# Kernel optimization log

Measured on AMD Instinct MI355X. Metric: run time of the kernel, lower is better.

## Reference

```python
import jax, jax.numpy as jnp
import numpy as np

HIDDEN = 4096
NUM_HEADS = 32
NUM_KV_HEADS = 8
HEAD_DIM = HIDDEN // NUM_HEADS  # 128
GROUPS = NUM_HEADS // NUM_KV_HEADS  # 4
ROPE_THETA = 10000.0


def setup_inputs() -> dict:
    key = jax.random.key(0)
    k0, k1, k2, k3, k4 = jax.random.split(key, 5)
    b, s = 2, 2048
    hidden_states = jax.random.normal(k0, (b, s, HIDDEN), dtype=jnp.float32)
    position_ids = jnp.broadcast_to(jnp.arange(s, dtype=jnp.int64), (b, s))
    sc = 1.0 / np.sqrt(HIDDEN)
    Wq = jax.random.normal(k1, (HIDDEN, NUM_HEADS * HEAD_DIM), dtype=jnp.float32) * sc
    Wk = jax.random.normal(k2, (HIDDEN, NUM_KV_HEADS * HEAD_DIM), dtype=jnp.float32) * sc
    Wv = jax.random.normal(k3, (HIDDEN, NUM_KV_HEADS * HEAD_DIM), dtype=jnp.float32) * sc
    Wo = jax.random.normal(k4, (NUM_HEADS * HEAD_DIM, HIDDEN), dtype=jnp.float32) * sc
    return {"hidden_states": hidden_states, "position_ids": position_ids,
            "Wq": Wq, "Wk": Wk, "Wv": Wv, "Wo": Wo}


def _rope(x, cos, sin):
    # x: [b, s, h, d]; cos/sin: [b, s, 1, d]
    d2 = x.shape[-1] // 2
    x1, x2 = x[..., :d2], x[..., d2:]
    rot = jnp.concatenate([-x2, x1], axis=-1)
    return x * cos + rot * sin


def reference(hidden_states, position_ids, Wq, Wk, Wv, Wo):
    b, s, _ = hidden_states.shape
    scale = 1.0 / np.sqrt(HEAD_DIM)
    # projections (Linear, no bias) kept in [b, s, h, d] layout
    q = (hidden_states @ Wq).reshape(b, s, NUM_HEADS, HEAD_DIM)
    k = (hidden_states @ Wk).reshape(b, s, NUM_KV_HEADS, HEAD_DIM)
    v = (hidden_states @ Wv).reshape(b, s, NUM_KV_HEADS, HEAD_DIM)
    # RoPE: emb = cat(freqs, freqs)
    inv_freq = 1.0 / (ROPE_THETA ** (jnp.arange(0, HEAD_DIM, 2, dtype=jnp.float32) / HEAD_DIM))
    freqs = position_ids.astype(jnp.float32)[..., None] * inv_freq  # [b, s, d/2]
    emb = jnp.concatenate([freqs, freqs], axis=-1)[:, :, None, :]   # [b, s, 1, d]
    cos, sin = jnp.cos(emb), jnp.sin(emb)
    q = _rope(q, cos, sin)
    k = _rope(k, cos, sin)
    # GQA: query head h maps to kv head h // GROUPS (repeat_kv is contiguous expand)
    qg = q.reshape(b, s, NUM_KV_HEADS, GROUPS, HEAD_DIM)
    scores = jnp.einsum('bqkgd,bskd->bkgqs', qg, k) * scale  # [b, kv, g, s_q, s_k]
    probs = jax.nn.softmax(scores, axis=-1)
    out = jnp.einsum('bkgqs,bskd->bqkgd', probs, v).reshape(b, s, HIDDEN)
    return out @ Wo
```

## Files before the change

### kernel.cpp

```cpp
#include <hip/hip_runtime.h>

typedef unsigned short u16;
typedef unsigned int u32;
typedef __attribute__((ext_vector_type(8))) __bf16 bf16x8;
typedef __attribute__((ext_vector_type(4))) float f32x4;
typedef __attribute__((ext_vector_type(4))) u32 u32x4;

__device__ __forceinline__ u16 f2bf(float f) {
  union { float f; u32 u; } v; v.f = f;
  u32 r = v.u + 0x7fffu + ((v.u >> 16) & 1u);
  return (u16)(r >> 16);
}
__device__ __forceinline__ float bf2f(u16 h) {
  return __uint_as_float(((u32)h) << 16);
}
__device__ __forceinline__ u32 pk2(float a, float b) {
  return (u32)f2bf(a) | ((u32)f2bf(b) << 16);
}
__device__ __forceinline__ void gld16(void* lds, const void* g) {
  __builtin_amdgcn_global_load_lds(
      (__attribute__((address_space(1))) void*)g,
      (__attribute__((address_space(3))) void*)lds, 16, 0, 0);
}

__global__ void convert_x(const float* __restrict__ src, u16* __restrict__ dst) {
  const size_t c = (size_t)blockIdx.x * blockDim.x + threadIdx.x;
  const float* s = src + c * 8;
  u16 t[8];
#pragma unroll
  for (int i = 0; i < 8; ++i) t[i] = f2bf(s[i]);
  ((uint4*)dst)[c] = *(const uint4*)t;
}

__global__ void transpose_w(const float* __restrict__ srcf, u16* __restrict__ dst,
                            int K, int N) {
  __shared__ u16 tile[64][72];
  const int r0 = blockIdx.y * 64, c0 = blockIdx.x * 64;
  const int tr = threadIdx.x >> 2;
  const int tc = (threadIdx.x & 3) * 16;
  const float* src = srcf + (size_t)(r0 + tr) * N + c0 + tc;
  u16* t = &tile[tr][tc];
#pragma unroll
  for (int i = 0; i < 16; ++i) t[i] = f2bf(src[i]);
  __syncthreads();
  u16 tmp[16];
#pragma unroll
  for (int i = 0; i < 16; ++i) tmp[i] = tile[tc + i][tr];
  uint4* gd = (uint4*)(dst + (size_t)(c0 + tr) * K + r0 + tc);
  gd[0] = *(uint4*)&tmp[0];
  gd[1] = *(uint4*)&tmp[8];
}

__global__ void transpose_v(const u16* __restrict__ V, u16* __restrict__ Vt) {
  __shared__ u16 tile[64][72];
  const int z = blockIdx.z, b = z >> 3, h = z & 7;
  const int s0 = blockIdx.y * 64;
  const int d0 = blockIdx.x * 64;
  const u16* src = V + ((size_t)(b * 2048 + s0)) * 1024 + h * 128 + d0;
  u16* dst = Vt + ((size_t)((b * 8 + h) * 128 + d0)) * 2048 + s0;
  const int tr = threadIdx.x >> 2;
  const int tc = (threadIdx.x & 3) * 16;
  const uint4* gs = (const uint4*)(src + (size_t)tr * 1024 + tc);
  *(uint4*)&tile[tr][tc] = gs[0];
  *(uint4*)&tile[tr][tc + 8] = gs[1];
  __syncthreads();
  u16 tmp[16];
#pragma unroll
  for (int i = 0; i < 16; ++i) tmp[i] = tile[tc + i][tr];
  uint4* gd = (uint4*)(dst + (size_t)tr * 2048 + tc);
  gd[0] = *(uint4*)&tmp[0];
  gd[1] = *(uint4*)&tmp[8];
}

template <int OUT32>
__global__ __launch_bounds__(256, 2) void gemm_bt128(
    const u16* __restrict__ A, const u16* __restrict__ Bt,
    void* __restrict__ Cv, int K, int N) {
  __shared__ u16 As[128 * 64];
  __shared__ u16 Bs[128 * 64];
  const int tid = threadIdx.x;
  const int wave = tid >> 6, lane = tid & 63;
  const int m0 = blockIdx.y * 128, n0 = blockIdx.x * 128;
  const int wr = (wave >> 1) * 64, wc = (wave & 1) * 64;
  const int lrow = lane & 15, quad = lane >> 4;
  const int cbase = wave * 64 + lane;

  f32x4 acc[4][4];
#pragma unroll
  for (int i = 0; i < 4; ++i)
#pragma unroll
    for (int j = 0; j < 4; ++j) acc[i][j] = (f32x4){0.f, 0.f, 0.f, 0.f};

  for (int k0 = 0; k0 < K; k0 += 64) {
#pragma unroll
    for (int r = 0; r < 4; ++r) {
      const int c = r * 256 + cbase;
      const int row = c >> 3, col = (c & 7) * 8;
      gld16(&As[(size_t)(r * 4 + wave) * 512],
            A + (size_t)(m0 + row) * K + k0 + col);
      gld16(&Bs[(size_t)(r * 4 + wave) * 512],
            Bt + (size_t)(n0 + row) * K + k0 + col);
    }
    __syncthreads();
#pragma unroll
    for (int kk = 0; kk < 2; ++kk) {
      const int ko = kk * 32 + quad * 8;
      bf16x8 af[4], bfr[4];
#pragma unroll
      for (int i = 0; i < 4; ++i)
        af[i] = *(const bf16x8*)&As[(wr + i * 16 + lrow) * 64 + ko];
#pragma unroll
      for (int j = 0; j < 4; ++j)
        bfr[j] = *(const bf16x8*)&Bs[(wc + j * 16 + lrow) * 64 + ko];
#pragma unroll
      for (int i = 0; i < 4; ++i)
#pragma unroll
        for (int j = 0; j < 4; ++j)
          acc[i][j] = __builtin_amdgcn_mfma_f32_16x16x32_bf16(af[i], bfr[j], acc[i][j], 0, 0, 0);
    }
    __syncthreads();
  }
#pragma unroll
  for (int i = 0; i < 4; ++i)
#pragma unroll
    for (int j = 0; j < 4; ++j)
#pragma unroll
      for (int reg = 0; reg < 4; ++reg) {
        const int row = m0 + wr + i * 16 + quad * 4 + reg;
        const int col = n0 + wc + j * 16 + lrow;
        if (OUT32)
          ((float*)Cv)[(size_t)row * N + col] = acc[i][j][reg];
        else
          ((u16*)Cv)[(size_t)row * N + col] = f2bf(acc[i][j][reg]);
      }
}

__global__ void rope_kernel(u16* __restrict__ Q, u16* __restrict__ Kc) {
  const int row = blockIdx.x;
  const float p = (float)(row & 2047);
  const float csc = 0.088388347762774597f * 1.4426950408889634f;
  for (int t = threadIdx.x; t < 2560; t += 256) {
    u16* base;
    int d;
    float sc;
    if (t < 2048) { const int h = t >> 6; d = t & 63; base = Q + (size_t)row * 4096 + h * 128; sc = csc; }
    else { const int tt = t - 2048; const int h = tt >> 6; d = tt & 63; base = Kc + (size_t)row * 1024 + h * 128; sc = 1.f; }
    const float inv = exp2f((float)d * -0.20762050593046807f);
    const float f = p * inv;
    float s, c;
    sincosf(f, &s, &c);
    const float x1 = bf2f(base[d]);
    const float x2 = bf2f(base[d + 64]);
    base[d] = f2bf((x1 * c - x2 * s) * sc);
    base[d + 64] = f2bf((x2 * c + x1 * s) * sc);
  }
}

__global__ __launch_bounds__(256, 3) void attn(
    const u16* __restrict__ Q, const u16* __restrict__ Kc,
    const u16* __restrict__ Vt, u16* __restrict__ O) {
  __shared__ u16 smem[16384];
  u16* Qs = smem;
  u16* Ks = smem;
  u16* Vs = smem + 8192;
  const int tid = threadIdx.x, wave = tid >> 6, lane = tid & 63;
  const int qt = blockIdx.x, qh = blockIdx.y, b = blockIdx.z;
  const int kvh = qh >> 2;
  const int lrow = lane & 15, quad = lane >> 4;
  const int swz = (lrow & 7) << 3;

  const u16* qb = Q + ((size_t)(b * 2048 + qt * 128)) * 4096 + qh * 128;
#pragma unroll
  for (int r = 0; r < 8; ++r) {
    const int c = (r * 4 + wave) * 64 + lane;
    const int row = c >> 4, scol = (c & 15) ^ (row & 7);
    gld16(&Qs[(size_t)(r * 4 + wave) * 512],
          qb + (size_t)row * 4096 + scol * 8);
  }
  __syncthreads();
  bf16x8 aq[2][4];
#pragma unroll
  for (int i = 0; i < 2; ++i)
#pragma unroll
    for (int kk = 0; kk < 4; ++kk)
      aq[i][kk] = *(const bf16x8*)
          &Qs[(wave * 32 + i * 16 + lrow) * 128 + ((kk * 32 + quad * 8) ^ swz)];
  __syncthreads();

  {
    const u16* kb = Kc + ((size_t)(b * 2048)) * 1024 + kvh * 128;
#pragma unroll
    for (int r = 0; r < 4; ++r) {
      const int c = (r * 4 + wave) * 64 + lane;
      const int m = c >> 4, scol = (c & 15) ^ (m & 7);
      const int srcrow = ((m >> 5) << 5) | (((m >> 2) & 3) << 3) |
                         (((m >> 4) & 1) << 2) | (m & 3);
      gld16(&Ks[(size_t)(r * 4 + wave) * 512],
            kb + (size_t)srcrow * 1024 + scol * 8);
    }
  }
  __syncthreads();

  f32x4 acco[2][8];
#pragma unroll
  for (int i = 0; i < 2; ++i)
#pragma unroll
    for (int j = 0; j < 8; ++j) acco[i][j] = (f32x4){0.f, 0.f, 0.f, 0.f};
  float m_i[2], l_i[2];
#pragma unroll
  for (int i = 0; i < 2; ++i) { m_i[i] = -INFINITY; l_i[i] = 0.f; }

  const u16* vbase = Vt + ((size_t)((b * 8 + kvh) * 128)) * 2048;

  for (int kv0 = 0; kv0 < 2048; kv0 += 64) {
#pragma unroll
    for (int r = 0; r < 4; ++r) {
      const int c = (r * 4 + wave) * 64 + lane;
      const int row = c >> 3, scol = (c & 7) ^ (row & 7);
      gld16(&Vs[(size_t)(r * 4 + wave) * 512],
            vbase + (size_t)row * 2048 + kv0 + scol * 8);
    }

    f32x4 s[2][4];
#pragma unroll
    for (int i = 0; i < 2; ++i)
#pragma unroll
      for (int j = 0; j < 4; ++j) s[i][j] = (f32x4){0.f, 0.f, 0.f, 0.f};
    __builtin_amdgcn_s_setprio(1);
#pragma unroll
    for (int kk = 0; kk < 4; ++kk) {
      const int ko = (kk * 32 + quad * 8) ^ swz;
#pragma unroll
      for (int j = 0; j < 4; ++j) {
        const bf16x8 bk = *(const bf16x8*)&Ks[(j * 16 + lrow) * 128 + ko];
        s[0][j] = __builtin_amdgcn_mfma_f32_16x16x32_bf16(bk, aq[0][kk], s[0][j], 0, 0, 0);
        s[1][j] = __builtin_amdgcn_mfma_f32_16x16x32_bf16(bk, aq[1][kk], s[1][j], 0, 0, 0);
      }
    }
    __builtin_amdgcn_s_setprio(0);

#pragma unroll
    for (int i = 0; i < 2; ++i) {
      float mx = s[i][0][0];
#pragma unroll
      for (int j = 0; j < 4; ++j)
#pragma unroll
        for (int reg = 0; reg < 4; ++reg) mx = fmaxf(mx, s[i][j][reg]);
      mx = fmaxf(mx, __shfl_xor(mx, 16));
      mx = fmaxf(mx, __shfl_xor(mx, 32));
      const bool grow = !__all(mx <= m_i[i] + 8.f);
      float mnew = m_i[i], al = 1.f;
      if (grow) {
        mnew = fmaxf(m_i[i], mx);
        al = exp2f(m_i[i] - mnew);
        m_i[i] = mnew;
      }
      float rs = 0.f;
#pragma unroll
      for (int j = 0; j < 4; ++j)
#pragma unroll
        for (int reg = 0; reg < 4; ++reg) {
          const float p0 = exp2f(s[i][j][reg] - mnew);
          s[i][j][reg] = p0;
          rs += p0;
        }
      rs += __shfl_xor(rs, 16);
      rs += __shfl_xor(rs, 32);
      l_i[i] = l_i[i] * al + rs;
      if (grow) {
#pragma unroll
        for (int j = 0; j < 8; ++j)
#pragma unroll
          for (int reg = 0; reg < 4; ++reg) acco[i][j][reg] *= al;
      }
    }

    u32x4 pw[2][2];
#pragma unroll
    for (int i = 0; i < 2; ++i)
#pragma unroll
      for (int kk = 0; kk < 2; ++kk) {
        pw[i][kk].x = pk2(s[i][2 * kk][0], s[i][2 * kk][1]);
        pw[i][kk].y = pk2(s[i][2 * kk][2], s[i][2 * kk][3]);
        pw[i][kk].z = pk2(s[i][2 * kk + 1][0], s[i][2 * kk + 1][1]);
        pw[i][kk].w = pk2(s[i][2 * kk + 1][2], s[i][2 * kk + 1][3]);
      }
    __syncthreads();

    if (kv0 + 64 < 2048) {
      const u16* kb = Kc + ((size_t)(b * 2048 + kv0 + 64)) * 1024 + kvh * 128;
#pragma unroll
      for (int r = 0; r < 4; ++r) {
        const int c = (r * 4 + wave) * 64 + lane;
        const int m = c >> 4, scol = (c & 15) ^ (m & 7);
        const int srcrow = ((m >> 5) << 5) | (((m >> 2) & 3) << 3) |
                           (((m >> 4) & 1) << 2) | (m & 3);
        gld16(&Ks[(size_t)(r * 4 + wave) * 512],
              kb + (size_t)srcrow * 1024 + scol * 8);
      }
    }

    __builtin_amdgcn_s_setprio(1);
#pragma unroll
    for (int kk = 0; kk < 2; ++kk) {
      const int kov = (kk * 32 + quad * 8) ^ swz;
      const bf16x8 ap0 = __builtin_bit_cast(bf16x8, pw[0][kk]);
      const bf16x8 ap1 = __builtin_bit_cast(bf16x8, pw[1][kk]);
#pragma unroll
      for (int j = 0; j < 8; ++j) {
        const bf16x8 bv = *(const bf16x8*)&Vs[(j * 16 + lrow) * 64 + kov];
        acco[0][j] = __builtin_amdgcn_mfma_f32_16x16x32_bf16(bv, ap0, acco[0][j], 0, 0, 0);
        acco[1][j] = __builtin_amdgcn_mfma_f32_16x16x32_bf16(bv, ap1, acco[1][j], 0, 0, 0);
      }
    }
    __builtin_amdgcn_s_setprio(0);
    __syncthreads();
  }

#pragma unroll
  for (int i = 0; i < 2; ++i) {
    const float inv = 1.0f / l_i[i];
    const int row = b * 2048 + qt * 128 + wave * 32 + i * 16 + lrow;
#pragma unroll
    for (int j = 0; j < 8; ++j) {
      u16 t4[4];
#pragma unroll
      for (int reg = 0; reg < 4; ++reg) t4[reg] = f2bf(acco[i][j][reg] * inv);
      *(uint2*)&O[(size_t)row * 4096 + qh * 128 + j * 16 + quad * 4] =
          *(const uint2*)t4;
    }
  }
}

extern "C" void kernel_launch(void* const* d_in, const int* in_sizes, int n_in,
                              void* d_out, int out_size, void* d_ws, size_t ws_size,
                              hipStream_t stream) {
  const float* X  = (const float*)d_in[0];
  const float* Wq = (const float*)d_in[2];
  const float* Wk = (const float*)d_in[3];
  const float* Wv = (const float*)d_in[4];
  const float* Wo = (const float*)d_in[5];
  u16* ws = (u16*)d_ws;

  u16* Xb = ws;
  u16* R0 = Xb + 16777216;
  u16* R1 = R0 + 16777216;
  u16* R2 = R1 + 16777216;
  u16* R3 = R2 + 4194304;
  u16* R4 = R3 + 4194304;
  u16* Qb = R1, *Kb = R3, *Vb = R4, *Vt = R2, *Ob = R0, *WoT = R1;

  convert_x<<<8192, 256, 0, stream>>>(X, Xb);

  transpose_w<<<dim3(64, 64), 256, 0, stream>>>(Wq, R0, 4096, 4096);
  gemm_bt128<0><<<dim3(32, 32), 256, 0, stream>>>(Xb, R0, Qb, 4096, 4096);

  transpose_w<<<dim3(16, 64), 256, 0, stream>>>(Wk, R0, 4096, 1024);
  gemm_bt128<0><<<dim3(8, 32), 256, 0, stream>>>(Xb, R0, Kb, 4096, 1024);

  transpose_w<<<dim3(16, 64), 256, 0, stream>>>(Wv, R0, 4096, 1024);
  gemm_bt128<0><<<dim3(8, 32), 256, 0, stream>>>(Xb, R0, Vb, 4096, 1024);

  rope_kernel<<<4096, 256, 0, stream>>>(Qb, Kb);
  transpose_v<<<dim3(2, 32, 16), 256, 0, stream>>>(Vb, Vt);

  attn<<<dim3(16, 32, 2), 256, 0, stream>>>(Qb, Kb, Vt, Ob);

  transpose_w<<<dim3(64, 64), 256, 0, stream>>>(Wo, WoT, 4096, 4096);
  gemm_bt128<1><<<dim3(32, 32), 256, 0, stream>>>(Ob, WoT, d_out, 4096, 4096);
}
```

Measured before the change: 1.065 ms.

## Batch K/V weight transpose and GEMM launches, stage attention output through LDS

Merges the K and V weight transposes into one launch and the K and V projection GEMMs into one 512-block launch, so each wave of the grid fills the GPU better than two 256-block launches. The attention kernel now stages its normalized output tile in shared memory and writes it back with coalesced 16-byte stores. The attention occupancy hint rises from 3 to 4 blocks per CU, with slightly more LDS per block, which may add register pressure.

```diff
diff --git a/kernel.cpp b/kernel.cpp
--- a/kernel.cpp
+++ b/kernel.cpp
@@ -35,6 +35,28 @@
 __global__ void transpose_w(const float* __restrict__ srcf, u16* __restrict__ dst,
                             int K, int N) {
   __shared__ u16 tile[64][72];
+  const int r0 = blockIdx.y * 64, c0 = blockIdx.x * 64;
+  const int tr = threadIdx.x >> 2;
+  const int tc = (threadIdx.x & 3) * 16;
+  const float* src = srcf + (size_t)(r0 + tr) * N + c0 + tc;
+  u16* t = &tile[tr][tc];
+#pragma unroll
+  for (int i = 0; i < 16; ++i) t[i] = f2bf(src[i]);
+  __syncthreads();
+  u16 tmp[16];
+#pragma unroll
+  for (int i = 0; i < 16; ++i) tmp[i] = tile[tc + i][tr];
+  uint4* gd = (uint4*)(dst + (size_t)(c0 + tr) * K + r0 + tc);
+  gd[0] = *(uint4*)&tmp[0];
+  gd[1] = *(uint4*)&tmp[8];
+}
+
+__global__ void transpose_w2(const float* __restrict__ s0, u16* __restrict__ d0,
+                             const float* __restrict__ s1, u16* __restrict__ d1,
+                             int K, int N) {
+  __shared__ u16 tile[64][72];
+  const float* srcf = blockIdx.z ? s1 : s0;
+  u16* dst = blockIdx.z ? d1 : d0;
   const int r0 = blockIdx.y * 64, c0 = blockIdx.x * 64;
   const int tr = threadIdx.x >> 2;
   const int tc = (threadIdx.x & 3) * 16;
@@ -73,14 +95,11 @@
 }
 
 template <int OUT32>
-__global__ __launch_bounds__(256, 2) void gemm_bt128(
-    const u16* __restrict__ A, const u16* __restrict__ Bt,
-    void* __restrict__ Cv, int K, int N) {
-  __shared__ u16 As[128 * 64];
-  __shared__ u16 Bs[128 * 64];
+__device__ __forceinline__ void gemm_body(
+    const u16* A, const u16* Bt, void* Cv, int K, int N, int m0, int n0,
+    u16* As, u16* Bs) {
   const int tid = threadIdx.x;
   const int wave = tid >> 6, lane = tid & 63;
-  const int m0 = blockIdx.y * 128, n0 = blockIdx.x * 128;
   const int wr = (wave >> 1) * 64, wc = (wave & 1) * 64;
   const int lrow = lane & 15, quad = lane >> 4;
   const int cbase = wave * 64 + lane;
@@ -133,6 +152,27 @@
         else
           ((u16*)Cv)[(size_t)row * N + col] = f2bf(acc[i][j][reg]);
       }
+}
+
+template <int OUT32>
+__global__ __launch_bounds__(256, 2) void gemm_bt128(
+    const u16* __restrict__ A, const u16* __restrict__ Bt,
+    void* __restrict__ Cv, int K, int N) {
+  __shared__ u16 As[128 * 64];
+  __shared__ u16 Bs[128 * 64];
+  gemm_body<OUT32>(A, Bt, Cv, K, N, blockIdx.y * 128, blockIdx.x * 128, As, Bs);
+}
+
+__global__ __launch_bounds__(256, 2) void gemm_kv(
+    const u16* __restrict__ A, const u16* __restrict__ KtW,
+    const u16* __restrict__ VtW, u16* __restrict__ Kb, u16* __restrict__ Vb,
+    int K, int N) {
+  __shared__ u16 As[128 * 64];
+  __shared__ u16 Bs[128 * 64];
+  const int sel = blockIdx.x >> 3;
+  const u16* Bt = sel ? VtW : KtW;
+  u16* C = sel ? Vb : Kb;
+  gemm_body<0>(A, Bt, C, K, N, blockIdx.y * 128, (blockIdx.x & 7) * 128, As, Bs);
 }
 
 __global__ void rope_kernel(u16* __restrict__ Q, u16* __restrict__ Kc) {
@@ -156,13 +196,14 @@
   }
 }
 
-__global__ __launch_bounds__(256, 3) void attn(
+__global__ __launch_bounds__(256, 4) void attn(
     const u16* __restrict__ Q, const u16* __restrict__ Kc,
     const u16* __restrict__ Vt, u16* __restrict__ O) {
-  __shared__ u16 smem[16384];
+  __shared__ u16 smem[17408];
   u16* Qs = smem;
   u16* Ks = smem;
   u16* Vs = smem + 8192;
+  u16* Os = smem;
   const int tid = threadIdx.x, wave = tid >> 6, lane = tid & 63;
   const int qt = blockIdx.x, qh = blockIdx.y, b = blockIdx.z;
   const int kvh = qh >> 2;
@@ -320,15 +361,23 @@
 #pragma unroll
   for (int i = 0; i < 2; ++i) {
     const float inv = 1.0f / l_i[i];
-    const int row = b * 2048 + qt * 128 + wave * 32 + i * 16 + lrow;
+    const int rl = wave * 32 + i * 16 + lrow;
 #pragma unroll
     for (int j = 0; j < 8; ++j) {
       u16 t4[4];
 #pragma unroll
       for (int reg = 0; reg < 4; ++reg) t4[reg] = f2bf(acco[i][j][reg] * inv);
-      *(uint2*)&O[(size_t)row * 4096 + qh * 128 + j * 16 + quad * 4] =
-          *(const uint2*)t4;
-    }
+      *(uint2*)&Os[rl * 136 + j * 16 + quad * 4] = *(const uint2*)t4;
+    }
+  }
+  __syncthreads();
+  const u16* obase = O + ((size_t)(b * 2048 + qt * 128)) * 4096 + qh * 128;
+#pragma unroll
+  for (int r = 0; r < 8; ++r) {
+    const int chunk = r * 256 + tid;
+    const int row = chunk >> 4, col = (chunk & 15) * 8;
+    *(uint4*)(const_cast<u16*>(obase) + (size_t)row * 4096 + col) =
+        *(const uint4*)&Os[row * 136 + col];
   }
 }
 
@@ -349,17 +398,16 @@
   u16* R3 = R2 + 4194304;
   u16* R4 = R3 + 4194304;
   u16* Qb = R1, *Kb = R3, *Vb = R4, *Vt = R2, *Ob = R0, *WoT = R1;
+  u16* WkT = R0;
+  u16* WvT = R0 + 4194304;
 
   convert_x<<<8192, 256, 0, stream>>>(X, Xb);
 
   transpose_w<<<dim3(64, 64), 256, 0, stream>>>(Wq, R0, 4096, 4096);
   gemm_bt128<0><<<dim3(32, 32), 256, 0, stream>>>(Xb, R0, Qb, 4096, 4096);
 
-  transpose_w<<<dim3(16, 64), 256, 0, stream>>>(Wk, R0, 4096, 1024);
-  gemm_bt128<0><<<dim3(8, 32), 256, 0, stream>>>(Xb, R0, Kb, 4096, 1024);
-
-  transpose_w<<<dim3(16, 64), 256, 0, stream>>>(Wv, R0, 4096, 1024);
-  gemm_bt128<0><<<dim3(8, 32), 256, 0, stream>>>(Xb, R0, Vb, 4096, 1024);
+  transpose_w2<<<dim3(16, 64, 2), 256, 0, stream>>>(Wk, WkT, Wv, WvT, 4096, 1024);
+  gemm_kv<<<dim3(16, 32), 256, 0, stream>>>(Xb, WkT, WvT, Kb, Vb, 4096, 1024);
 
   rope_kernel<<<4096, 256, 0, stream>>>(Qb, Kb);
   transpose_v<<<dim3(2, 32, 16), 256, 0, stream>>>(Vb, Vt);
```

Result: slower. 1.215 ms (+14.1%).
